# Kernel tuning notes

Hardware: AMD Instinct MI355X
Metric: run time of the kernel (lower is better)

The kernel has to match this reference:

```python
import jax, jax.numpy as jnp
import numpy as np

B = 2; N_RAW = 16384; N_KP = 2048; M_VOX = 8192; C_VOX = 64
H_BEV, W_BEV, C_BEV, BEV_STRIDE = 200, 176, 256, 8
VOXEL_SIZE = np.array([0.05, 0.05, 0.1], np.float32)
PC_MIN = np.array([0.0, -40.0, -3.0], np.float32)
DOWNSAMPLE = 4
RAW_RADII = (0.4, 0.8); RAW_NS = (16, 16)
CONV_RADII = (1.2, 2.4); CONV_NS = (16, 32)
BN_SCALE = float(1.0 / np.sqrt(1.0 + 1e-5))  # eval-mode BN, running mean=0 var=1


def _fps_idx(pts, n):
    # farthest point sampling over pts [N,3] -> [n] int32 indices
    N = pts.shape[0]
    def step(carry, _):
        dists, last = carry
        d = jnp.sum((pts - pts[last]) ** 2, axis=-1)
        dists = jnp.minimum(dists, d)
        nxt = jnp.argmax(dists).astype(jnp.int32)
        return (dists, nxt), nxt
    init = (jnp.full((N,), 1e10, pts.dtype), jnp.int32(0))
    _, rest = jax.lax.scan(step, init, None, length=n - 1)
    return jnp.concatenate([jnp.zeros((1,), jnp.int32), rest])


def _bilinear(bev, x, y):
    # bev [H,W,C]; faithful to bilinear_interpolate_bev (clamp then weight)
    H, W, _ = bev.shape
    xf = jnp.floor(x); yf = jnp.floor(y)
    x0 = jnp.clip(xf.astype(jnp.int32), 0, W - 1)
    x1 = jnp.clip(xf.astype(jnp.int32) + 1, 0, W - 1)
    y0 = jnp.clip(yf.astype(jnp.int32), 0, H - 1)
    y1 = jnp.clip(yf.astype(jnp.int32) + 1, 0, H - 1)
    fa = bev[y1, x0]; fb = bev[y1, x1]; fc = bev[y0, x1]; fd = bev[y0, x0]
    x0f = x0.astype(x.dtype); x1f = x1.astype(x.dtype)
    y0f = y0.astype(y.dtype); y1f = y1.astype(y.dtype)
    wa = (x - x0f) * (y1f - y); wb = (x1f - x) * (y1f - y)
    wc = (x1f - x) * (y - y0f); wd = (x - x0f) * (y - y0f)
    return fd * wb[:, None] + fc * wa[:, None] + fa * wc[:, None] + fb * wd[:, None]


def _group(xyz, feats, new_xyz, radius, nsample):
    # ball query: first nsample points within radius (original order), pad with first hit
    M = xyz.shape[0]
    d2 = jnp.sum((new_xyz[:, None, :] - xyz[None, :, :]) ** 2, axis=-1)  # [K,M]
    mask = d2 < radius * radius
    key = jnp.where(mask, jnp.arange(M, dtype=jnp.int32)[None, :], M)
    idx = jnp.sort(key, axis=1)[:, :nsample]
    empty = ~jnp.any(mask, axis=1)
    idx = jnp.where(idx < M, idx, idx[:, :1])
    idx = jnp.clip(idx, 0, M - 1)
    g_xyz = xyz[idx] - new_xyz[:, None, :]
    g = jnp.concatenate([g_xyz, feats[idx]], axis=-1)  # [K,ns,3+C]
    return jnp.where(empty[:, None, None], 0.0, g), empty


def _bn_relu(x, g, b):
    return jax.nn.relu(x * (g * BN_SCALE) + b)


def _sa(xyz, feats, new_xyz, radii, nss, w0, g0, b0, w1, g1, b1):
    outs = []
    for i, (r, ns) in enumerate(zip(radii, nss)):
        grouped, empty = jax.vmap(lambda x, f, nx: _group(x, f, nx, r, ns))(xyz, feats, new_xyz)
        h = _bn_relu(grouped @ w0[i], g0[i], b0[i])
        h = _bn_relu(h @ w1[i], g1[i], b1[i])
        pooled = jnp.max(h, axis=2)  # [B,K,Cout]
        outs.append(jnp.where(empty[..., None], 0.0, pooled))
    return jnp.concatenate(outs, axis=-1)


def _forward(points, spatial_features, voxel_coords, voxel_features,
             raw_w0, raw_g0, raw_b0, raw_w1, raw_g1, raw_b1,
             conv_w0, conv_g0, conv_b0, conv_w1, conv_g1, conv_b1,
             fusion_w, fusion_g, fusion_b):
    pts = points.reshape(B, N_RAW, -1)
    xyz_raw = pts[..., 1:4]
    idxs = jax.vmap(lambda p: _fps_idx(p, N_KP))(jax.lax.stop_gradient(xyz_raw))
    kp = jnp.take_along_axis(xyz_raw, idxs[..., None], axis=1)  # [B,NKP,3]
    xi = (kp[..., 0] - PC_MIN[0]) / VOXEL_SIZE[0] / BEV_STRIDE
    yi = (kp[..., 1] - PC_MIN[1]) / VOXEL_SIZE[1] / BEV_STRIDE
    bev = jnp.transpose(spatial_features, (0, 2, 3, 1))  # [B,H,W,C]
    bev_feat = jax.vmap(_bilinear)(bev, xi, yi)  # [B,NKP,C_BEV]
    raw_feat = _sa(xyz_raw, pts[..., 4:], kp, RAW_RADII, RAW_NS,
                   raw_w0, raw_g0, raw_b0, raw_w1, raw_g1, raw_b1)
    vc = voxel_coords.reshape(B, M_VOX, 4)
    centers = (vc[..., jnp.array([3, 2, 1])].astype(jnp.float32) + 0.5) \
        * jnp.asarray(VOXEL_SIZE * DOWNSAMPLE) + jnp.asarray(PC_MIN)
    conv_feat = _sa(centers, voxel_features.reshape(B, M_VOX, C_VOX), kp, CONV_RADII, CONV_NS,
                    conv_w0, conv_g0, conv_b0, conv_w1, conv_g1, conv_b1)
    feats = jnp.concatenate([bev_feat, raw_feat, conv_feat], axis=-1).reshape(B * N_KP, -1)
    return _bn_relu(feats @ fusion_w, fusion_g, fusion_b)  # [B*NKP, 128]


def setup_inputs():
    key = jax.random.key(0)
    ks = jax.random.split(key, 8)
    xyz = jax.random.uniform(ks[0], (B * N_RAW, 3), jnp.float32) * jnp.array([70.4, 80.0, 4.0]) + jnp.array([0.0, -40.0, -3.0])
    inten = jax.random.uniform(ks[1], (B * N_RAW, 1), jnp.float32)
    bidx = jnp.repeat(jnp.arange(B, dtype=jnp.float32), N_RAW)[:, None]
    points = jnp.concatenate([bidx, xyz, inten], axis=1)
    spatial_features = jax.random.normal(ks[2], (B, C_BEV, H_BEV, W_BEV), jnp.float32)
    vb = jnp.repeat(jnp.arange(B, dtype=jnp.int32), M_VOX)[:, None]
    vz = jax.random.randint(ks[3], (B * M_VOX, 1), 0, 10, jnp.int32)
    vy = jax.random.randint(ks[4], (B * M_VOX, 1), 0, 400, jnp.int32)
    vx = jax.random.randint(ks[5], (B * M_VOX, 1), 0, 352, jnp.int32)
    voxel_coords = jnp.concatenate([vb, vz, vy, vx], axis=1)
    voxel_features = jax.random.normal(ks[6], (B * M_VOX, C_VOX), jnp.float32)
    pk = jax.random.split(ks[7], 5)
    w = lambda k, s: jax.random.normal(k, s, jnp.float32) * 0.05
    return dict(
        points=points, spatial_features=spatial_features,
        voxel_coords=voxel_coords, voxel_features=voxel_features,
        raw_w0=w(pk[0], (2, 4, 16)), raw_g0=jnp.ones((2, 16)), raw_b0=jnp.zeros((2, 16)),
        raw_w1=w(pk[1], (2, 16, 16)), raw_g1=jnp.ones((2, 16)), raw_b1=jnp.zeros((2, 16)),
        conv_w0=w(pk[2], (2, 67, 64)), conv_g0=jnp.ones((2, 64)), conv_b0=jnp.zeros((2, 64)),
        conv_w1=w(pk[3], (2, 64, 64)), conv_g1=jnp.ones((2, 64)), conv_b1=jnp.zeros((2, 64)),
        fusion_w=w(pk[4], (416, 128)), fusion_g=jnp.ones((128,)), fusion_b=jnp.zeros((128,)))


def reference(points, spatial_features, voxel_coords, voxel_features,
              raw_w0, raw_g0, raw_b0, raw_w1, raw_g1, raw_b1,
              conv_w0, conv_g0, conv_b0, conv_w1, conv_g1, conv_b1,
              fusion_w, fusion_g, fusion_b):
    return _forward(points, spatial_features, voxel_coords, voxel_features,
                    raw_w0, raw_g0, raw_b0, raw_w1, raw_g1, raw_b1,
                    conv_w0, conv_g0, conv_b0, conv_w1, conv_g1, conv_b1,
                    fusion_w, fusion_g, fusion_b)
```

## Files before the change

kernel.cpp:

```cpp
#include <hip/hip_runtime.h>


#define NRAW   16384
#define MVOX   8192
#define NKP    2048
#define NKPALL 4096

__device__ __constant__ float kBNS = (float)0.9999950000374997;

__global__ __launch_bounds__(256) void prep_kernel(
    const float* __restrict__ pts, const int* __restrict__ vc,
    float4* __restrict__ xyz4, float4* __restrict__ cxyz4) {
#pragma clang fp contract(off)
  int i = blockIdx.x * 256 + threadIdx.x;
  if (i < 2 * NRAW) {
    const float* p = pts + (size_t)i * 5;
    xyz4[i] = make_float4(p[1], p[2], p[3], p[4]);
  }
  if (i < 2 * MVOX) {
    const int* v = vc + (size_t)i * 4;
    cxyz4[i] = make_float4(((float)v[3] + 0.5f) * 0.2f + 0.0f,
                           ((float)v[2] + 0.5f) * 0.2f + -40.0f,
                           ((float)v[1] + 0.5f) * 0.4f + -3.0f, 0.f);
  }
}

__global__ __launch_bounds__(1024) void sort_kernel(
    const float* __restrict__ pts, int* __restrict__ sperm) {
  const int b = blockIdx.x, t = threadIdx.x;
  __shared__ unsigned hist[256], cur[256];
  if (t < 256) hist[t] = 0u;
  __syncthreads();
  int bins[16];
#pragma unroll
  for (int k = 0; k < 16; ++k) {
    const int i = k * 1024 + t;
    const float y = pts[(size_t)(b * NRAW + i) * 5 + 2];
    int bin = (int)((y + 40.0f) * 3.2f);
    bin = bin < 0 ? 0 : (bin > 255 ? 255 : bin);
    bins[k] = bin;
    atomicAdd(&hist[bin], 1u);
  }
  __syncthreads();
  if (t == 0) {
    unsigned acc = 0;
    for (int i = 0; i < 256; ++i) { cur[i] = acc; acc += hist[i]; }
  }
  __syncthreads();
#pragma unroll
  for (int k = 0; k < 16; ++k) {
    const int i = k * 1024 + t;
    const unsigned pos = atomicAdd(&cur[bins[k]], 1u);
    sperm[b * NRAW + pos] = i;
  }
}

__device__ __forceinline__ unsigned wave_umax63(unsigned v) {
  unsigned t;
  t = (unsigned)__builtin_amdgcn_update_dpp(0, (int)v, 0xB1,  0xf, 0xf, true); v = v < t ? t : v;
  t = (unsigned)__builtin_amdgcn_update_dpp(0, (int)v, 0x4E,  0xf, 0xf, true); v = v < t ? t : v;
  t = (unsigned)__builtin_amdgcn_update_dpp(0, (int)v, 0x124, 0xf, 0xf, true); v = v < t ? t : v;
  t = (unsigned)__builtin_amdgcn_update_dpp(0, (int)v, 0x128, 0xf, 0xf, true); v = v < t ? t : v;
  t = (unsigned)__builtin_amdgcn_update_dpp(0, (int)v, 0x142, 0xa, 0xf, true); v = v < t ? t : v;
  t = (unsigned)__builtin_amdgcn_update_dpp(0, (int)v, 0x143, 0xc, 0xf, true); v = v < t ? t : v;
  return v;
}

__global__ __launch_bounds__(1024, 4) void fps_kernel(
    const int* __restrict__ sperm, const float4* __restrict__ xyz4,
    float* __restrict__ kx, float* __restrict__ ky, float* __restrict__ kz) {
#pragma clang fp contract(off)
  const int b = blockIdx.x;
  const int t = threadIdx.x;
  const int w = t >> 6, lane = t & 63;
  const int wb = w * 1024;
  const int base = b * NRAW;

  __shared__ unsigned long long slot[3];

  int pj[16];
  float px[16], py[16], pz[16], dd[16];
#pragma unroll
  for (int j = 0; j < 16; ++j)
    pj[j] = sperm[base + wb + j * 64 + lane];
#pragma unroll
  for (int j = 0; j < 16; ++j) {
    const float4 q = xyz4[base + pj[j]];
    px[j] = q.x; py[j] = q.y; pz[j] = q.z; dd[j] = 1e10f;
  }
  if (t < 3) slot[t] = 0ULL;

  float bnx = px[0], bxx = px[0], bny = py[0], bxy = py[0], bnz = pz[0], bxz = pz[0];
#pragma unroll
  for (int j = 1; j < 16; ++j) {
    bnx = fminf(bnx, px[j]); bxx = fmaxf(bxx, px[j]);
    bny = fminf(bny, py[j]); bxy = fmaxf(bxy, py[j]);
    bnz = fminf(bnz, pz[j]); bxz = fmaxf(bxz, pz[j]);
  }
#pragma unroll
  for (int off = 1; off < 64; off <<= 1) {
    bnx = fminf(bnx, __shfl_xor(bnx, off, 64));
    bxx = fmaxf(bxx, __shfl_xor(bxx, off, 64));
    bny = fminf(bny, __shfl_xor(bny, off, 64));
    bxy = fmaxf(bxy, __shfl_xor(bxy, off, 64));
    bnz = fminf(bnz, __shfl_xor(bnz, off, 64));
    bxz = fmaxf(bxz, __shfl_xor(bxz, off, 64));
  }

  const float4 p0 = xyz4[base];
  float lx = p0.x, ly = p0.y, lz = p0.z;
  if (t == 0) { kx[b * NKP] = lx; ky[b * NKP] = ly; kz[b * NKP] = lz; }

  unsigned long long cpk = 0ULL;
  float bvc = __builtin_inff();
  __syncthreads();

  for (int s = 1; s < NKP; ++s) {
    float dxm = fmaxf(fmaxf(bnx - lx, lx - bxx), 0.f);
    float dym = fmaxf(fmaxf(bny - ly, ly - bxy), 0.f);
    float dzm = fmaxf(fmaxf(bnz - lz, lz - bxz), 0.f);
    const float LB2 = dxm * dxm + dym * dym + dzm * dzm;
    if (!(LB2 * 0.9999f > bvc)) {
#pragma unroll
      for (int j = 0; j < 16; ++j) {
        float dx = px[j] - lx, dy = py[j] - ly, dz = pz[j] - lz;
        float d2 = dx * dx; d2 = d2 + dy * dy; d2 = d2 + dz * dz;
        dd[j] = fminf(dd[j], d2);
      }
      float m8[8];
#pragma unroll
      for (int j = 0; j < 8; ++j) m8[j] = fmaxf(dd[2 * j], dd[2 * j + 1]);
      float m4[4];
#pragma unroll
      for (int j = 0; j < 4; ++j) m4[j] = fmaxf(m8[2 * j], m8[2 * j + 1]);
      const float bv = fmaxf(fmaxf(m4[0], m4[1]), fmaxf(m4[2], m4[3]));

      const unsigned vb = __float_as_uint(bv);
      const unsigned wmax =
          (unsigned)__builtin_amdgcn_readlane((int)wave_umax63(vb), 63);
      unsigned mo = 0xFFFFFFFFu;
      if (vb == wmax) {
#pragma unroll
        for (int j = 0; j < 16; ++j)
          if (__float_as_uint(dd[j]) == wmax) {
            const unsigned o = (unsigned)pj[j];
            mo = o < mo ? o : mo;
          }
      }
      const unsigned cand = (vb == wmax) ? ~mo : 0u;
      const unsigned cm =
          (unsigned)__builtin_amdgcn_readlane((int)wave_umax63(cand), 63);
      cpk = ((unsigned long long)wmax << 32) | (unsigned long long)cm;
      bvc = __uint_as_float(wmax);
    }
    if (lane == 63) atomicMax(&slot[s % 3], cpk);
    __syncthreads();

    const unsigned long long g = slot[s % 3];
    const int wi = __builtin_amdgcn_readfirstlane((int)~(unsigned)g);
    if (t == 0) slot[(s + 2) % 3] = 0ULL;
    const float4 cw = xyz4[base + wi];
    lx = cw.x; ly = cw.y; lz = cw.z;
    if (t == 0) { kx[b * NKP + s] = lx; ky[b * NKP + s] = ly; kz[b * NKP + s] = lz; }
  }
}

__global__ __launch_bounds__(256) void bev_kernel(
    const float* __restrict__ sf, const float* __restrict__ kx,
    const float* __restrict__ ky, float* __restrict__ feats) {
#pragma clang fp contract(off)
  const int kidx = blockIdx.x;
  const int c = threadIdx.x;
  const int b = kidx >> 11;
  const float x = (kx[kidx] - 0.0f) / 0.05f / 8.0f;
  const float y = (ky[kidx] - (-40.0f)) / 0.05f / 8.0f;
  const float xf = floorf(x), yf = floorf(y);
  int x0 = (int)xf;     x0 = x0 < 0 ? 0 : (x0 > 175 ? 175 : x0);
  int x1 = (int)xf + 1; x1 = x1 < 0 ? 0 : (x1 > 175 ? 175 : x1);
  int y0 = (int)yf;     y0 = y0 < 0 ? 0 : (y0 > 199 ? 199 : y0);
  int y1 = (int)yf + 1; y1 = y1 < 0 ? 0 : (y1 > 199 ? 199 : y1);
  const float x0f = (float)x0, x1f = (float)x1, y0f = (float)y0, y1f = (float)y1;
  const float wa = (x - x0f) * (y1f - y);
  const float wb = (x1f - x) * (y1f - y);
  const float wc = (x1f - x) * (y - y0f);
  const float wd = (x - x0f) * (y - y0f);
  const float* base = sf + ((size_t)b * 256 + c) * (200 * 176);
  const float fa = base[y1 * 176 + x0];
  const float fb = base[y1 * 176 + x1];
  const float fc = base[y0 * 176 + x1];
  const float fd = base[y0 * 176 + x0];
  float r = fd * wb; r = r + fc * wa; r = r + fa * wc; r = r + fb * wd;
  feats[(size_t)kidx * 416 + c] = r;
}

__global__ __launch_bounds__(256) void raw_sa_kernel(
    const float4* __restrict__ xyz4,
    const float* __restrict__ kx, const float* __restrict__ ky,
    const float* __restrict__ kz,
    const float* __restrict__ w0, const float* __restrict__ g0,
    const float* __restrict__ b0, const float* __restrict__ w1,
    const float* __restrict__ g1, const float* __restrict__ b1,
    float* __restrict__ feats) {
  const int wv = threadIdx.x >> 6;
  const int lane = threadIdx.x & 63;
  const int gw = blockIdx.x * 4 + wv;
  const int ri = gw >> 12;
  const int kidx = gw & 4095;
  const int b = kidx >> 11;
  const float R2 = ri ? (float)(0.8 * 0.8) : (float)(0.4 * 0.4);

  __shared__ int   idxl[4][16];
  __shared__ float hbuf[4][16][17];

  const float kxv = kx[kidx], kyv = ky[kidx], kzv = kz[kidx];
  const int base = b * NRAW;
  int cnt = 0;
  {
#pragma clang fp contract(off)
    for (int ch = 0; ch < NRAW / 64 && cnt < 16; ++ch) {
      const float4 q = xyz4[base + ch * 64 + lane];
      float dx = kxv - q.x, dy = kyv - q.y, dz = kzv - q.z;
      float d2 = dx * dx; d2 = d2 + dy * dy; d2 = d2 + dz * dz;
      unsigned long long m = __ballot(d2 < R2);
      while (m && cnt < 16) {
        int bit = __builtin_ctzll(m);
        if (lane == 0) idxl[wv][cnt] = ch * 64 + bit;
        ++cnt;
        m &= m - 1;
      }
    }
  }
  const int outoff = kidx * 416 + 256 + ri * 16;
  if (cnt == 0) {
    if (lane < 16) feats[outoff + lane] = 0.f;
    return;
  }
  __threadfence_block();

  const int s = lane & 15, cq = lane >> 4;
  const int ss = (s < cnt) ? s : 0;
  const float4 q = xyz4[base + idxl[wv][ss]];
  const float gx = q.x - kxv, gy = q.y - kyv, gz = q.z - kzv, gi = q.w;
  const int wb0 = ri * 64, cb = ri * 16;
#pragma unroll
  for (int j = 0; j < 4; ++j) {
    int c = cq * 4 + j;
    float a = gx * w0[wb0 + c];
    a = fmaf(gy, w0[wb0 + 16 + c], a);
    a = fmaf(gz, w0[wb0 + 32 + c], a);
    a = fmaf(gi, w0[wb0 + 48 + c], a);
    a = fmaf(a, g0[cb + c] * kBNS, b0[cb + c]);
    hbuf[wv][s][c] = fmaxf(a, 0.f);
  }
  __threadfence_block();
  float o0 = 0.f, o1 = 0.f, o2 = 0.f, o3 = 0.f;
  const int wb1 = ri * 256;
#pragma unroll
  for (int k = 0; k < 16; ++k) {
    float hk = hbuf[wv][s][k];
    o0 = fmaf(hk, w1[wb1 + k * 16 + cq * 4 + 0], o0);
    o1 = fmaf(hk, w1[wb1 + k * 16 + cq * 4 + 1], o1);
    o2 = fmaf(hk, w1[wb1 + k * 16 + cq * 4 + 2], o2);
    o3 = fmaf(hk, w1[wb1 + k * 16 + cq * 4 + 3], o3);
  }
  float v0 = fmaxf(fmaf(o0, g1[cb + cq * 4 + 0] * kBNS, b1[cb + cq * 4 + 0]), 0.f);
  float v1 = fmaxf(fmaf(o1, g1[cb + cq * 4 + 1] * kBNS, b1[cb + cq * 4 + 1]), 0.f);
  float v2 = fmaxf(fmaf(o2, g1[cb + cq * 4 + 2] * kBNS, b1[cb + cq * 4 + 2]), 0.f);
  float v3 = fmaxf(fmaf(o3, g1[cb + cq * 4 + 3] * kBNS, b1[cb + cq * 4 + 3]), 0.f);
#pragma unroll
  for (int off = 1; off < 16; off <<= 1) {
    v0 = fmaxf(v0, __shfl_xor(v0, off, 64));
    v1 = fmaxf(v1, __shfl_xor(v1, off, 64));
    v2 = fmaxf(v2, __shfl_xor(v2, off, 64));
    v3 = fmaxf(v3, __shfl_xor(v3, off, 64));
  }
  if (s == 0) {
    feats[outoff + cq * 4 + 0] = v0;
    feats[outoff + cq * 4 + 1] = v1;
    feats[outoff + cq * 4 + 2] = v2;
    feats[outoff + cq * 4 + 3] = v3;
  }
}

__global__ __launch_bounds__(256) void conv_sa_kernel(
    const float4* __restrict__ cxyz4, const float* __restrict__ vf,
    const float* __restrict__ kx, const float* __restrict__ ky,
    const float* __restrict__ kz,
    const float* __restrict__ w0, const float* __restrict__ g0,
    const float* __restrict__ b0, const float* __restrict__ w1,
    const float* __restrict__ g1, const float* __restrict__ b1,
    float* __restrict__ feats) {
  const int wv = threadIdx.x >> 6;
  const int lane = threadIdx.x & 63;
  const int gw = blockIdx.x * 4 + wv;
  const int ri = gw >> 12;
  const int kidx = gw & 4095;
  const int b = kidx >> 11;
  const int NS = ri ? 32 : 16;
  const float R2 = ri ? (float)(2.4 * 2.4) : (float)(1.2 * 1.2);

  __shared__ int   idxl[4][32];
  __shared__ float gbuf[4][64];
  __shared__ float hbuf[4][32][64];

  const float kxv = kx[kidx], kyv = ky[kidx], kzv = kz[kidx];
  const int base = b * MVOX;
  int cnt = 0;
  {
#pragma clang fp contract(off)
    for (int ch = 0; ch < MVOX / 64 && cnt < NS; ++ch) {
      const float4 q = cxyz4[base + ch * 64 + lane];
      float dx = kxv - q.x, dy = kyv - q.y, dz = kzv - q.z;
      float d2 = dx * dx; d2 = d2 + dy * dy; d2 = d2 + dz * dz;
      unsigned long long m = __ballot(d2 < R2);
      while (m && cnt < NS) {
        int bit = __builtin_ctzll(m);
        if (lane == 0) idxl[wv][cnt] = ch * 64 + bit;
        ++cnt;
        m &= m - 1;
      }
    }
  }
  const int outoff = kidx * 416 + 288 + ri * 64;
  if (cnt == 0) {
    feats[outoff + lane] = 0.f;
    return;
  }
  __threadfence_block();

  const float wA0 = w0[(ri * 67 + 0) * 64 + lane];
  const float wA1 = w0[(ri * 67 + 1) * 64 + lane];
  const float wA2 = w0[(ri * 67 + 2) * 64 + lane];
  float wB[64];
#pragma unroll
  for (int k = 0; k < 64; ++k) wB[k] = w0[(ri * 67 + 3 + k) * 64 + lane];
  float wC[64];
#pragma unroll
  for (int k = 0; k < 64; ++k) wC[k] = w1[(ri * 64 + k) * 64 + lane];
  const float s0 = g0[ri * 64 + lane] * kBNS, bb0 = b0[ri * 64 + lane];
  const float s1 = g1[ri * 64 + lane] * kBNS, bb1 = b1[ri * 64 + lane];

  for (int sm = 0; sm < cnt; ++sm) {
    const int p = base + idxl[wv][sm];
    const float4 q = cxyz4[p];
    const float ox = q.x - kxv, oy = q.y - kyv, oz = q.z - kzv;
    gbuf[wv][lane] = vf[(size_t)p * 64 + lane];
    __threadfence_block();
    float acc = ox * wA0;
    acc = fmaf(oy, wA1, acc);
    acc = fmaf(oz, wA2, acc);
#pragma unroll
    for (int k4 = 0; k4 < 16; ++k4) {
      float4 g4 = *(const float4*)&gbuf[wv][k4 * 4];
      acc = fmaf(g4.x, wB[k4 * 4 + 0], acc);
      acc = fmaf(g4.y, wB[k4 * 4 + 1], acc);
      acc = fmaf(g4.z, wB[k4 * 4 + 2], acc);
      acc = fmaf(g4.w, wB[k4 * 4 + 3], acc);
    }
    hbuf[wv][sm][lane] = fmaxf(fmaf(acc, s0, bb0), 0.f);
    __threadfence_block();
  }
  float mx = -1e30f;
  for (int sm = 0; sm < cnt; ++sm) {
    float acc = 0.f;
#pragma unroll
    for (int k4 = 0; k4 < 16; ++k4) {
      float4 h4 = *(const float4*)&hbuf[wv][sm][k4 * 4];
      acc = fmaf(h4.x, wC[k4 * 4 + 0], acc);
      acc = fmaf(h4.y, wC[k4 * 4 + 1], acc);
      acc = fmaf(h4.z, wC[k4 * 4 + 2], acc);
      acc = fmaf(h4.w, wC[k4 * 4 + 3], acc);
    }
    mx = fmaxf(mx, fmaxf(fmaf(acc, s1, bb1), 0.f));
  }
  feats[outoff + lane] = mx;
}

__global__ __launch_bounds__(256) void fusion_kernel(
    const float* __restrict__ feats, const float* __restrict__ fw,
    const float* __restrict__ fg, const float* __restrict__ fb,
    float* __restrict__ out) {
  const int gid = blockIdx.x * 256 + threadIdx.x;
  const int kidx = gid >> 7, c = gid & 127;
  const float* f = feats + (size_t)kidx * 416;
  float acc = 0.f;
#pragma unroll 4
  for (int k = 0; k < 416; k += 4) {
    float4 fv = *(const float4*)(f + k);
    acc = fmaf(fv.x, fw[(k + 0) * 128 + c], acc);
    acc = fmaf(fv.y, fw[(k + 1) * 128 + c], acc);
    acc = fmaf(fv.z, fw[(k + 2) * 128 + c], acc);
    acc = fmaf(fv.w, fw[(k + 3) * 128 + c], acc);
  }
  out[gid] = fmaxf(fmaf(acc, fg[c] * kBNS, fb[c]), 0.f);
}

extern "C" void kernel_launch(void* const* d_in, const int* in_sizes, int n_in,
                              void* d_out, int out_size, void* d_ws, size_t ws_size,
                              hipStream_t stream) {
  (void)in_sizes; (void)n_in; (void)out_size; (void)ws_size;
  const float* pts = (const float*)d_in[0];
  const float* sf  = (const float*)d_in[1];
  const int*   vc  = (const int*)d_in[2];
  const float* vf  = (const float*)d_in[3];
  const float* raw_w0 = (const float*)d_in[4];
  const float* raw_g0 = (const float*)d_in[5];
  const float* raw_b0 = (const float*)d_in[6];
  const float* raw_w1 = (const float*)d_in[7];
  const float* raw_g1 = (const float*)d_in[8];
  const float* raw_b1 = (const float*)d_in[9];
  const float* conv_w0 = (const float*)d_in[10];
  const float* conv_g0 = (const float*)d_in[11];
  const float* conv_b0 = (const float*)d_in[12];
  const float* conv_w1 = (const float*)d_in[13];
  const float* conv_g1 = (const float*)d_in[14];
  const float* conv_b1 = (const float*)d_in[15];
  const float* fus_w = (const float*)d_in[16];
  const float* fus_g = (const float*)d_in[17];
  const float* fus_b = (const float*)d_in[18];
  float* out = (float*)d_out;

  float* W = (float*)d_ws;
  float4* xyz4  = (float4*)W;
  float4* cxyz4 = (float4*)(W + 131072);
  float* kx    = W + 196608;
  float* ky    = W + 200704;
  float* kz    = W + 204800;
  float* feats = W + 208896;
  int* sperm = (int*)(W + 208896);

  prep_kernel<<<128, 256, 0, stream>>>(pts, vc, xyz4, cxyz4);
  sort_kernel<<<2, 1024, 0, stream>>>(pts, sperm);
  fps_kernel<<<2, 1024, 0, stream>>>(sperm, xyz4, kx, ky, kz);
  bev_kernel<<<NKPALL, 256, 0, stream>>>(sf, kx, ky, feats);
  raw_sa_kernel<<<2048, 256, 0, stream>>>(xyz4, kx, ky, kz,
                                          raw_w0, raw_g0, raw_b0, raw_w1, raw_g1, raw_b1,
                                          feats);
  conv_sa_kernel<<<2048, 256, 0, stream>>>(cxyz4, vf, kx, ky, kz,
                                           conv_w0, conv_g0, conv_b0, conv_w1, conv_g1, conv_b1,
                                           feats);
  fusion_kernel<<<2048, 256, 0, stream>>>(feats, fus_w, fus_g, fus_b, out);
}
```

Baseline: 2.371 ms.

## Add per-chunk bounding-box pruning and LDS candidate table to FPS loop

Splits each wave's 16 points per lane into four chunks with their own bounding boxes and cached maxima. A chunk's distances are updated only if the new point could reduce them, and the wave argmax is skipped when no chunk changed. Each wave also writes its candidate coordinates to a shared table, so the next point is read from LDS instead of a dependent global load of xyz4. This adds branching, extra registers and a wave-index encoding in the atomic key.

```diff
diff --git a/kernel.cpp b/kernel.cpp
--- a/kernel.cpp
+++ b/kernel.cpp
@@ -70,19 +70,17 @@
     const int* __restrict__ sperm, const float4* __restrict__ xyz4,
     float* __restrict__ kx, float* __restrict__ ky, float* __restrict__ kz) {
 #pragma clang fp contract(off)
-  const int b = blockIdx.x;
-  const int t = threadIdx.x;
+  const int b = blockIdx.x, t = threadIdx.x;
   const int w = t >> 6, lane = t & 63;
-  const int wb = w * 1024;
-  const int base = b * NRAW;
+  const int wb = w * 1024, base = b * NRAW;
 
   __shared__ unsigned long long slot[3];
+  __shared__ float4 tabC[3][16];
 
   int pj[16];
   float px[16], py[16], pz[16], dd[16];
 #pragma unroll
-  for (int j = 0; j < 16; ++j)
-    pj[j] = sperm[base + wb + j * 64 + lane];
+  for (int j = 0; j < 16; ++j) pj[j] = sperm[base + wb + j * 64 + lane];
 #pragma unroll
   for (int j = 0; j < 16; ++j) {
     const float4 q = xyz4[base + pj[j]];
@@ -90,76 +88,105 @@
   }
   if (t < 3) slot[t] = 0ULL;
 
-  float bnx = px[0], bxx = px[0], bny = py[0], bxy = py[0], bnz = pz[0], bxz = pz[0];
-#pragma unroll
-  for (int j = 1; j < 16; ++j) {
-    bnx = fminf(bnx, px[j]); bxx = fmaxf(bxx, px[j]);
-    bny = fminf(bny, py[j]); bxy = fmaxf(bxy, py[j]);
-    bnz = fminf(bnz, pz[j]); bxz = fmaxf(bxz, pz[j]);
-  }
-#pragma unroll
-  for (int off = 1; off < 64; off <<= 1) {
-    bnx = fminf(bnx, __shfl_xor(bnx, off, 64));
-    bxx = fmaxf(bxx, __shfl_xor(bxx, off, 64));
-    bny = fminf(bny, __shfl_xor(bny, off, 64));
-    bxy = fmaxf(bxy, __shfl_xor(bxy, off, 64));
-    bnz = fminf(bnz, __shfl_xor(bnz, off, 64));
-    bxz = fmaxf(bxz, __shfl_xor(bxz, off, 64));
-  }
+  float cbnx[4], cbxx[4], cbny[4], cbxy[4], cbnz[4], cbxz[4], cmaxL[4];
+#pragma unroll
+  for (int c = 0; c < 4; ++c) {
+    float nx = px[4 * c], xx = nx, ny = py[4 * c], xy = ny, nz = pz[4 * c], xz = nz;
+#pragma unroll
+    for (int j = 4 * c + 1; j < 4 * c + 4; ++j) {
+      nx = fminf(nx, px[j]); xx = fmaxf(xx, px[j]);
+      ny = fminf(ny, py[j]); xy = fmaxf(xy, py[j]);
+      nz = fminf(nz, pz[j]); xz = fmaxf(xz, pz[j]);
+    }
+#pragma unroll
+    for (int off = 1; off < 64; off <<= 1) {
+      nx = fminf(nx, __shfl_xor(nx, off, 64)); xx = fmaxf(xx, __shfl_xor(xx, off, 64));
+      ny = fminf(ny, __shfl_xor(ny, off, 64)); xy = fmaxf(xy, __shfl_xor(xy, off, 64));
+      nz = fminf(nz, __shfl_xor(nz, off, 64)); xz = fmaxf(xz, __shfl_xor(xz, off, 64));
+    }
+    cbnx[c] = nx; cbxx[c] = xx; cbny[c] = ny; cbxy[c] = xy; cbnz[c] = nz; cbxz[c] = xz;
+    cmaxL[c] = 1e10f;
+  }
+  const float wnx = fminf(fminf(cbnx[0], cbnx[1]), fminf(cbnx[2], cbnx[3]));
+  const float wxx = fmaxf(fmaxf(cbxx[0], cbxx[1]), fmaxf(cbxx[2], cbxx[3]));
+  const float wny = fminf(fminf(cbny[0], cbny[1]), fminf(cbny[2], cbny[3]));
+  const float wxy = fmaxf(fmaxf(cbxy[0], cbxy[1]), fmaxf(cbxy[2], cbxy[3]));
+  const float wnz = fminf(fminf(cbnz[0], cbnz[1]), fminf(cbnz[2], cbnz[3]));
+  const float wxz = fmaxf(fmaxf(cbxz[0], cbxz[1]), fmaxf(cbxz[2], cbxz[3]));
 
   const float4 p0 = xyz4[base];
   float lx = p0.x, ly = p0.y, lz = p0.z;
   if (t == 0) { kx[b * NKP] = lx; ky[b * NKP] = ly; kz[b * NKP] = lz; }
 
-  unsigned long long cpk = 0ULL;
+  unsigned long long cpk = ((unsigned long long)w << 1) | 1ULL;
+  float ccx = lx, ccy = ly, ccz = lz;
   float bvc = __builtin_inff();
   __syncthreads();
 
   for (int s = 1; s < NKP; ++s) {
-    float dxm = fmaxf(fmaxf(bnx - lx, lx - bxx), 0.f);
-    float dym = fmaxf(fmaxf(bny - ly, ly - bxy), 0.f);
-    float dzm = fmaxf(fmaxf(bnz - lz, lz - bxz), 0.f);
-    const float LB2 = dxm * dxm + dym * dym + dzm * dzm;
-    if (!(LB2 * 0.9999f > bvc)) {
-#pragma unroll
-      for (int j = 0; j < 16; ++j) {
-        float dx = px[j] - lx, dy = py[j] - ly, dz = pz[j] - lz;
-        float d2 = dx * dx; d2 = d2 + dy * dy; d2 = d2 + dz * dz;
-        dd[j] = fminf(dd[j], d2);
+    const int buf = s % 3;
+    float dxm = fmaxf(fmaxf(wnx - lx, lx - wxx), 0.f);
+    float dym = fmaxf(fmaxf(wny - ly, ly - wxy), 0.f);
+    float dzm = fmaxf(fmaxf(wnz - lz, lz - wxz), 0.f);
+    const float LB2w = dxm * dxm + dym * dym + dzm * dzm;
+    if (!(LB2w * 0.9999f > bvc)) {
+      bool any = false;
+#pragma unroll
+      for (int c = 0; c < 4; ++c) {
+        float cdx = fmaxf(fmaxf(cbnx[c] - lx, lx - cbxx[c]), 0.f);
+        float cdy = fmaxf(fmaxf(cbny[c] - ly, ly - cbxy[c]), 0.f);
+        float cdz = fmaxf(fmaxf(cbnz[c] - lz, lz - cbxz[c]), 0.f);
+        const float LB2c = cdx * cdx + cdy * cdy + cdz * cdz;
+        if (__any(!(LB2c * 0.9999f > cmaxL[c]))) {
+          any = true;
+#pragma unroll
+          for (int j = 4 * c; j < 4 * c + 4; ++j) {
+            float dx = px[j] - lx, dy = py[j] - ly, dz = pz[j] - lz;
+            float d2 = dx * dx; d2 = d2 + dy * dy; d2 = d2 + dz * dz;
+            dd[j] = fminf(dd[j], d2);
+          }
+          cmaxL[c] = fmaxf(fmaxf(dd[4 * c], dd[4 * c + 1]),
+                           fmaxf(dd[4 * c + 2], dd[4 * c + 3]));
+        }
       }
-      float m8[8];
-#pragma unroll
-      for (int j = 0; j < 8; ++j) m8[j] = fmaxf(dd[2 * j], dd[2 * j + 1]);
-      float m4[4];
-#pragma unroll
-      for (int j = 0; j < 4; ++j) m4[j] = fmaxf(m8[2 * j], m8[2 * j + 1]);
-      const float bv = fmaxf(fmaxf(m4[0], m4[1]), fmaxf(m4[2], m4[3]));
-
-      const unsigned vb = __float_as_uint(bv);
-      const unsigned wmax =
-          (unsigned)__builtin_amdgcn_readlane((int)wave_umax63(vb), 63);
-      unsigned mo = 0xFFFFFFFFu;
-      if (vb == wmax) {
-#pragma unroll
-        for (int j = 0; j < 16; ++j)
-          if (__float_as_uint(dd[j]) == wmax) {
-            const unsigned o = (unsigned)pj[j];
-            mo = o < mo ? o : mo;
+      if (any) {
+        const float bv = fmaxf(fmaxf(cmaxL[0], cmaxL[1]), fmaxf(cmaxL[2], cmaxL[3]));
+        const unsigned vb = __float_as_uint(bv);
+        const unsigned wmax =
+            (unsigned)__builtin_amdgcn_readlane((int)wave_umax63(vb), 63);
+        const bool tied = (vb == wmax);
+        unsigned mo = 0xFFFFFFFFu;
+        float qx = 0.f, qy = 0.f, qz = 0.f;
+        if (tied) {
+#pragma unroll
+          for (int j = 0; j < 16; ++j) {
+            const bool hit = (__float_as_uint(dd[j]) == wmax) && ((unsigned)pj[j] < mo);
+            mo = hit ? (unsigned)pj[j] : mo;
+            qx = hit ? px[j] : qx; qy = hit ? py[j] : qy; qz = hit ? pz[j] : qz;
           }
+        }
+        const unsigned inv = tied ? (16383u - mo) : 0u;
+        const unsigned im =
+            (unsigned)__builtin_amdgcn_readlane((int)wave_umax63(inv), 63);
+        const unsigned mo_w = 16383u - im;
+        const unsigned long long mball = __ballot(tied && mo == mo_w);
+        const int l = __builtin_ctzll(mball);
+        ccx = __shfl(qx, l, 64); ccy = __shfl(qy, l, 64); ccz = __shfl(qz, l, 64);
+        cpk = ((unsigned long long)wmax << 32) | ((unsigned long long)im << 5) |
+              ((unsigned long long)w << 1) | 1ULL;
+        bvc = __uint_as_float(wmax);
       }
-      const unsigned cand = (vb == wmax) ? ~mo : 0u;
-      const unsigned cm =
-          (unsigned)__builtin_amdgcn_readlane((int)wave_umax63(cand), 63);
-      cpk = ((unsigned long long)wmax << 32) | (unsigned long long)cm;
-      bvc = __uint_as_float(wmax);
-    }
-    if (lane == 63) atomicMax(&slot[s % 3], cpk);
+    }
+    if (lane == 63) {
+      atomicMax(&slot[buf], cpk);
+      tabC[buf][w] = make_float4(ccx, ccy, ccz, 0.f);
+    }
     __syncthreads();
 
-    const unsigned long long g = slot[s % 3];
-    const int wi = __builtin_amdgcn_readfirstlane((int)~(unsigned)g);
+    const unsigned long long g = slot[buf];
+    const int wid = (int)((g >> 1) & 0xFULL);
     if (t == 0) slot[(s + 2) % 3] = 0ULL;
-    const float4 cw = xyz4[base + wi];
+    const float4 cw = tabC[buf][wid];
     lx = cw.x; ly = cw.y; lz = cw.z;
     if (t == 0) { kx[b * NKP + s] = lx; ky[b * NKP + s] = ly; kz[b * NKP + s] = lz; }
   }
```

Result: slower. 7.208 ms (+204.0%).
